# Kernel optimization log

Hardware: AMD Instinct MI355X
Metric: run time of the kernel (lower is better)

## Reference

```python
import jax, jax.numpy as jnp
import numpy as np


def setup_inputs() -> dict:
    key = jax.random.key(0)
    k1, k2 = jax.random.split(key)
    x = jax.random.normal(k1, (64, 64, 32, 32), dtype=jnp.float32)
    codebook = jax.random.normal(k2, (1024, 64), dtype=jnp.float32)
    return {"x": x, "codebook": codebook}


def reference(x, codebook):
    B, C, H, W = x.shape
    # NCHW -> NHWC -> [N, C] flat tokens
    xt = jnp.transpose(x, (0, 2, 3, 1)).reshape(-1, C)  # [N, C]
    # squared euclidean distances [N, K] (argmin of squared == argmin of cdist)
    x_sq = jnp.sum(xt * xt, axis=-1, keepdims=True)          # [N, 1]
    cb_sq = jnp.sum(codebook * codebook, axis=-1)            # [K]
    d2 = x_sq - 2.0 * (xt @ codebook.T) + cb_sq[None, :]     # [N, K]
    idx_emb = jnp.argmin(d2, axis=-1)                        # [N]
    quant = codebook[idx_emb]                                # [N, C]
    loss_embed = jnp.mean((jax.lax.stop_gradient(xt) - quant) ** 2)
    loss_commitment = jnp.mean((xt - jax.lax.stop_gradient(quant)) ** 2)
    # straight-through estimator
    quant_out = xt + jax.lax.stop_gradient(quant - xt)
    quant_out = quant_out.reshape(B, H, W, C).transpose(0, 3, 1, 2)
    idx_emb = idx_emb.reshape(B, H * W)
    return quant_out, loss_embed, loss_commitment, idx_emb
```

## Files before the change

kernel.cpp:

```cpp
#include <hip/hip_runtime.h>

#define THREADS 256
#define M_BLOCK 128
#define C_DIM 64
#define K_CODES 1024
#define N_CHUNK 64
#define N_CHUNKS 16

#define QUANT_OFF 0
#define LOSS_OFF  4194304
#define IDX_OFF   4194306

#define WS_CBSQH_F 16
#define WS_STREAM_B 8192
#define CHUNK_BYTES 24576
#define SEG_BYTES 1024
#define WS_NEEDED (WS_STREAM_B + N_CHUNKS * CHUNK_BYTES)

typedef float floatx16 __attribute__((ext_vector_type(16)));
typedef short bf16x8  __attribute__((ext_vector_type(8)));

typedef __attribute__((address_space(1))) const void gv_t;
typedef __attribute__((address_space(3))) void lv_t;

static __device__ inline unsigned short f2bf(float v) {
    unsigned int u = __float_as_uint(v);
    unsigned int r = (u + 0x7FFF + ((u >> 16) & 1)) >> 16;
    return (unsigned short)r;
}
static __device__ inline float bf2f(unsigned short b) {
    return __uint_as_float(((unsigned int)b) << 16);
}

__global__ void vq_prep(const float* __restrict__ cb, float* __restrict__ ws)
{
    const int tid = threadIdx.x;
    if (blockIdx.x >= 96) {
        int code = (blockIdx.x - 96) * 256 + tid;
        const float4* row = reinterpret_cast<const float4*>(cb + code * C_DIM);
        float s = 0.f;
        #pragma unroll
        for (int j = 0; j < 16; ++j) {
            float4 v = row[j];
            s = fmaf(v.x, v.x, s); s = fmaf(v.y, v.y, s);
            s = fmaf(v.z, v.z, s); s = fmaf(v.w, v.w, s);
        }
        ws[WS_CBSQH_F + code] = 0.5f * s;
        return;
    }
    int gid   = blockIdx.x * 256 + tid;
    int chunk = gid / 1536;
    int rem   = gid - chunk * 1536;
    int seg   = rem >> 6;
    int lane  = rem & 63;
    int wc = seg / 12;
    int tb = (seg % 12) >> 2;
    int s4 = seg & 3;
    int code = chunk * N_CHUNK + wc * 32 + (lane & 31);
    int c0   = s4 * 16 + ((lane >> 5) << 3);
    const float* src = cb + code * C_DIM + c0;
    unsigned short us[8];
    #pragma unroll
    for (int j = 0; j < 8; ++j) {
        float v  = src[j];
        float h  = bf2f(f2bf(v));
        float r1 = v - h;
        float m  = bf2f(f2bf(r1));
        float r2 = r1 - m;
        float sel = (tb == 0) ? h : (tb == 1) ? m : r2;
        us[j] = f2bf(-sel);
    }
    uint4 o;
    o.x = (unsigned)us[0] | ((unsigned)us[1] << 16);
    o.y = (unsigned)us[2] | ((unsigned)us[3] << 16);
    o.z = (unsigned)us[4] | ((unsigned)us[5] << 16);
    o.w = (unsigned)us[6] | ((unsigned)us[7] << 16);
    *reinterpret_cast<uint4*>((char*)ws + WS_STREAM_B + chunk * CHUNK_BYTES
                              + seg * SEG_BYTES + lane * 16) = o;
}

__global__ __launch_bounds__(THREADS, 2) void vq_main(
    const float* __restrict__ x,
    const float* __restrict__ cb,
    const float* __restrict__ ws_f,
    float* __restrict__ out,
    double* __restrict__ ws_sum)
{
    __shared__ __align__(16) char smem[49152];
    __shared__ float cbsqh_s[K_CODES];
    __shared__ float redv[2][M_BLOCK];
    __shared__ int   redi[2][M_BLOCK];
    __shared__ int   kidx_s[M_BLOCK];

    const int tid  = threadIdx.x;
    const int blk  = blockIdx.x;
    const int tok0 = blk * M_BLOCK;
    const int b    = tok0 >> 10;
    const int hw0  = tok0 & 1023;

    const int w   = tid >> 6;
    const int ln  = tid & 63;
    const int wr  = w >> 1;
    const int wc  = w & 1;
    const int l31 = ln & 31;
    const int l5  = ln >> 5;

    float* xs = reinterpret_cast<float*>(smem);
    #pragma unroll
    for (int j = 0; j < 32; ++j) {
        int idx = j * 256 + tid;
        int c = idx >> 7, t = idx & 127;
        xs[c * 130 + t] = x[((b * C_DIM + c) << 10) + hw0 + t];
    }
    #pragma unroll
    for (int r = 0; r < 4; ++r) {
        int q = r * 256 + tid;
        cbsqh_s[q] = ws_f[WS_CBSQH_F + q];
    }
    __syncthreads();

    bf16x8 afrag[2][3][4];
    #pragma unroll
    for (int mt = 0; mt < 2; ++mt) {
        const int token = wr * 64 + mt * 32 + l31;
        #pragma unroll
        for (int s4 = 0; s4 < 4; ++s4) {
            const int cb0 = s4 * 16 + l5 * 8;
            #pragma unroll
            for (int j = 0; j < 8; ++j) {
                float v  = xs[(cb0 + j) * 130 + token];
                float h  = bf2f(f2bf(v));
                float r1 = v - h;
                float m  = bf2f(f2bf(r1));
                float r2 = r1 - m;
                afrag[mt][0][s4][j] = (short)f2bf(h);
                afrag[mt][1][s4][j] = (short)f2bf(m);
                afrag[mt][2][s4][j] = (short)f2bf(r2);
            }
        }
    }
    __syncthreads();

    const char* stream = (const char*)ws_f + WS_STREAM_B;

    {
        char* buf = smem;
        #pragma unroll
        for (int it = 0; it < 6; ++it) {
            int seg = w * 6 + it;
            const char* g = stream + 0 * CHUNK_BYTES + seg * SEG_BYTES + ln * 16;
            __builtin_amdgcn_global_load_lds((gv_t*)g, (lv_t*)(buf + seg * SEG_BYTES), 16, 0, 0);
        }
    }
    __syncthreads();

    float minv[2][16];
    int   mini[2][16];
    #pragma unroll
    for (int mt = 0; mt < 2; ++mt)
        #pragma unroll
        for (int r = 0; r < 16; ++r) { minv[mt][r] = 3.4e38f; mini[mt][r] = 0; }

    for (int ch = 0; ch < N_CHUNKS; ++ch) {
        if (ch < N_CHUNKS - 1) {
            char* nbuf = smem + ((ch + 1) & 1) * CHUNK_BYTES;
            #pragma unroll
            for (int it = 0; it < 6; ++it) {
                int seg = w * 6 + it;
                const char* g = stream + (ch + 1) * CHUNK_BYTES + seg * SEG_BYTES + ln * 16;
                __builtin_amdgcn_global_load_lds((gv_t*)g, (lv_t*)(nbuf + seg * SEG_BYTES), 16, 0, 0);
            }
        }

        const char* bbase = smem + (ch & 1) * CHUNK_BYTES;
        const float h = cbsqh_s[ch * N_CHUNK + wc * 32 + l31];
        floatx16 acc0, acc1;
        #pragma unroll
        for (int r = 0; r < 16; ++r) { acc0[r] = h; acc1[r] = h; }

        #pragma unroll
        for (int tb = 0; tb < 3; ++tb) {
            #pragma unroll
            for (int s4 = 0; s4 < 4; ++s4) {
                bf16x8 bf = *reinterpret_cast<const bf16x8*>(
                    bbase + ((wc * 3 + tb) * 4 + s4) * SEG_BYTES + ln * 16);
                #pragma unroll
                for (int a = 0; a < 3; ++a) {
                    if (a + tb <= 2) {
                        acc0 = __builtin_amdgcn_mfma_f32_32x32x16_bf16(afrag[0][a][s4], bf, acc0, 0, 0, 0);
                        acc1 = __builtin_amdgcn_mfma_f32_32x32x16_bf16(afrag[1][a][s4], bf, acc1, 0, 0, 0);
                    }
                }
            }
        }

        const int idxc = ch * N_CHUNK + wc * 32 + l31;
        #pragma unroll
        for (int r = 0; r < 16; ++r) {
            float s0 = acc0[r];
            if (s0 < minv[0][r]) { minv[0][r] = s0; mini[0][r] = idxc; }
            float s1 = acc1[r];
            if (s1 < minv[1][r]) { minv[1][r] = s1; mini[1][r] = idxc; }
        }
        __syncthreads();
    }

    #pragma unroll
    for (int off = 1; off < 32; off <<= 1) {
        #pragma unroll
        for (int mt = 0; mt < 2; ++mt)
            #pragma unroll
            for (int r = 0; r < 16; ++r) {
                float ov = __shfl_xor(minv[mt][r], off, 64);
                int   oi = __shfl_xor(mini[mt][r], off, 64);
                if (ov < minv[mt][r] || (ov == minv[mt][r] && oi < mini[mt][r])) {
                    minv[mt][r] = ov; mini[mt][r] = oi;
                }
            }
    }
    if (l31 == 0) {
        #pragma unroll
        for (int mt = 0; mt < 2; ++mt)
            #pragma unroll
            for (int r = 0; r < 16; ++r) {
                int row = (r & 3) + ((r >> 2) << 3) + (l5 << 2);
                int token = wr * 64 + mt * 32 + row;
                redv[wc][token] = minv[mt][r];
                redi[wc][token] = mini[mt][r];
            }
    }
    __syncthreads();

    if (tid < M_BLOCK) {
        float v0 = redv[0][tid]; int i0 = redi[0][tid];
        float v1 = redv[1][tid]; int i1 = redi[1][tid];
        int bi = (v1 < v0 || (v1 == v0 && i1 < i0)) ? i1 : i0;
        kidx_s[tid] = bi;
        out[IDX_OFF + tok0 + tid] = (float)bi;
    }
    __syncthreads();

    {
        const int i  = tid & (M_BLOCK - 1);
        const int c0 = tid >> 7;
        const int kk = kidx_s[i];
        const float* crow = cb + kk * C_DIM;
        float lsum = 0.f;
        #pragma unroll
        for (int j = 0; j < 32; ++j) {
            int c = c0 * 32 + j;
            float q  = crow[c];
            float xv = x[((b * C_DIM + c) << 10) + hw0 + i];
            float d  = q - xv;
            lsum = fmaf(d, d, lsum);
            out[QUANT_OFF + ((b * C_DIM + c) << 10) + hw0 + i] = xv + d;
        }
        #pragma unroll
        for (int off = 32; off > 0; off >>= 1)
            lsum += __shfl_down(lsum, off, 64);
        if ((tid & 63) == 0)
            atomicAdd(ws_sum, (double)lsum);
    }
}

#define CB_PAD 68
__global__ __launch_bounds__(THREADS, 2) void vq_main_valu(
    const float* __restrict__ x,
    const float* __restrict__ cb,
    float* __restrict__ out,
    double* __restrict__ ws_sum)
{
    __shared__ float xt_s[C_DIM][M_BLOCK];
    __shared__ float cb_s[C_DIM][CB_PAD];
    __shared__ float cbsq_all[K_CODES];
    __shared__ float red_v[8][M_BLOCK];
    __shared__ int   red_i[8][M_BLOCK];
    __shared__ int   kidx_s[M_BLOCK];

    const int tid  = threadIdx.x;
    const int tok0 = blockIdx.x * M_BLOCK;
    const int b_img = tok0 >> 10;
    const int hw0   = tok0 & 1023;

    #pragma unroll
    for (int r = 0; r < 4; ++r) {
        int k = tid + r * THREADS;
        const float4* row = reinterpret_cast<const float4*>(cb + k * C_DIM);
        float s = 0.f;
        #pragma unroll
        for (int j = 0; j < 16; ++j) {
            float4 v = row[j];
            s = fmaf(v.x, v.x, s); s = fmaf(v.y, v.y, s);
            s = fmaf(v.z, v.z, s); s = fmaf(v.w, v.w, s);
        }
        cbsq_all[k] = s;
    }
    {
        const int i  = tid & (M_BLOCK - 1);
        const int c0 = tid >> 7;
        #pragma unroll
        for (int j = 0; j < 32; ++j) {
            int c = c0 + 2 * j;
            xt_s[c][i] = x[((b_img * C_DIM + c) << 10) + hw0 + i];
        }
    }

    const int tl = tid & 31;
    const int kg = tid >> 5;
    float minv[4]; int mini[4];
    #pragma unroll
    for (int m = 0; m < 4; ++m) { minv[m] = 3.4e38f; mini[m] = 0; }

    for (int ch = 0; ch < 16; ++ch) {
        __syncthreads();
        for (int t = tid; t < 64 * C_DIM; t += THREADS) {
            int kl = t >> 6, c = t & 63;
            cb_s[c][kl] = cb[(ch * 64 + kl) * C_DIM + c];
        }
        __syncthreads();
        float dot[4][8];
        #pragma unroll
        for (int m = 0; m < 4; ++m)
            #pragma unroll
            for (int k = 0; k < 8; ++k) dot[m][k] = 0.f;
        #pragma unroll 4
        for (int c = 0; c < C_DIM; ++c) {
            float4 xv  = *reinterpret_cast<const float4*>(&xt_s[c][tl * 4]);
            float4 cv0 = *reinterpret_cast<const float4*>(&cb_s[c][kg * 8]);
            float4 cv1 = *reinterpret_cast<const float4*>(&cb_s[c][kg * 8 + 4]);
            float xa[4] = {xv.x, xv.y, xv.z, xv.w};
            float ca[8] = {cv0.x, cv0.y, cv0.z, cv0.w, cv1.x, cv1.y, cv1.z, cv1.w};
            #pragma unroll
            for (int m = 0; m < 4; ++m)
                #pragma unroll
                for (int k = 0; k < 8; ++k)
                    dot[m][k] = fmaf(xa[m], ca[k], dot[m][k]);
        }
        const int codebase = ch * 64 + kg * 8;
        #pragma unroll
        for (int k = 0; k < 8; ++k) {
            float csq = cbsq_all[codebase + k];
            #pragma unroll
            for (int m = 0; m < 4; ++m) {
                float sc = fmaf(-2.f, dot[m][k], csq);
                if (sc < minv[m]) { minv[m] = sc; mini[m] = codebase + k; }
            }
        }
    }
    #pragma unroll
    for (int m = 0; m < 4; ++m) {
        red_v[kg][tl * 4 + m] = minv[m];
        red_i[kg][tl * 4 + m] = mini[m];
    }
    __syncthreads();
    if (tid < M_BLOCK) {
        float bv = red_v[0][tid]; int bi = red_i[0][tid];
        #pragma unroll
        for (int g = 1; g < 8; ++g) {
            float v = red_v[g][tid]; int ii = red_i[g][tid];
            if (v < bv || (v == bv && ii < bi)) { bv = v; bi = ii; }
        }
        kidx_s[tid] = bi;
        out[IDX_OFF + tok0 + tid] = (float)bi;
    }
    __syncthreads();
    {
        const int i  = tid & (M_BLOCK - 1);
        const int c0 = tid >> 7;
        const int kk = kidx_s[i];
        const float* crow = cb + kk * C_DIM;
        float lsum = 0.f;
        #pragma unroll
        for (int j = 0; j < 32; ++j) {
            int c = c0 * 32 + j;
            float q  = crow[c];
            float xv = xt_s[c][i];
            float d  = q - xv;
            lsum = fmaf(d, d, lsum);
            out[QUANT_OFF + ((b_img * C_DIM + c) << 10) + hw0 + i] = xv + d;
        }
        #pragma unroll
        for (int off = 32; off > 0; off >>= 1)
            lsum += __shfl_down(lsum, off, 64);
        if ((tid & 63) == 0)
            atomicAdd(ws_sum, (double)lsum);
    }
}

__global__ void vq_finalize(const double* __restrict__ ws_sum,
                            float* __restrict__ out)
{
    float m = (float)(ws_sum[0] / 4194304.0);
    out[LOSS_OFF]     = m;
    out[LOSS_OFF + 1] = m;
}

extern "C" void kernel_launch(void* const* d_in, const int* in_sizes, int n_in,
                              void* d_out, int out_size, void* d_ws, size_t ws_size,
                              hipStream_t stream) {
    const float* x  = (const float*)d_in[0];
    const float* cb = (const float*)d_in[1];
    float* out      = (float*)d_out;

    hipMemsetAsync(d_ws, 0, sizeof(double), stream);
    if (ws_size >= (size_t)WS_NEEDED) {
        vq_prep<<<100, THREADS, 0, stream>>>(cb, (float*)d_ws);
        vq_main<<<512, THREADS, 0, stream>>>(x, cb, (const float*)d_ws, out, (double*)d_ws);
    } else {
        vq_main_valu<<<512, THREADS, 0, stream>>>(x, cb, out, (double*)d_ws);
    }
    vq_finalize<<<1, 1, 0, stream>>>((const double*)d_ws, out);
}
```

Before: 147.5 us.

## Stream codebook fragments directly to registers and drop LDS double buffering

The main kernel no longer stages codebook chunks in LDS through global_load_lds with per-chunk barriers. Each wave now loads its B fragments straight from global memory into registers, using two register sets (bA/bB) that are software-pipelined across pairs of chunks. The epilogue reads x from the retained LDS tile instead of re-reading global memory, and the prep kernel is relaunched with 64-thread blocks. This removes LDS traffic and block-wide syncs, but it adds register pressure (24 extra bf16x8 vectors) that may hurt occupancy at 2 waves/SIMD, and it relies on L2 for codebook reuse.

```diff
diff --git a/kernel.cpp b/kernel.cpp
--- a/kernel.cpp
+++ b/kernel.cpp
@@ -20,9 +20,6 @@
 typedef float floatx16 __attribute__((ext_vector_type(16)));
 typedef short bf16x8  __attribute__((ext_vector_type(8)));
 
-typedef __attribute__((address_space(1))) const void gv_t;
-typedef __attribute__((address_space(3))) void lv_t;
-
 static __device__ inline unsigned short f2bf(float v) {
     unsigned int u = __float_as_uint(v);
     unsigned int r = (u + 0x7FFF + ((u >> 16) & 1)) >> 16;
@@ -35,8 +32,9 @@
 __global__ void vq_prep(const float* __restrict__ cb, float* __restrict__ ws)
 {
     const int tid = threadIdx.x;
-    if (blockIdx.x >= 96) {
-        int code = (blockIdx.x - 96) * 256 + tid;
+    const int blk = blockIdx.x;
+    if (blk >= 384) {
+        int code = (blk - 384) * 64 + tid;
         const float4* row = reinterpret_cast<const float4*>(cb + code * C_DIM);
         float s = 0.f;
         #pragma unroll
@@ -48,16 +46,14 @@
         ws[WS_CBSQH_F + code] = 0.5f * s;
         return;
     }
-    int gid   = blockIdx.x * 256 + tid;
-    int chunk = gid / 1536;
-    int rem   = gid - chunk * 1536;
-    int seg   = rem >> 6;
-    int lane  = rem & 63;
-    int wc = seg / 12;
-    int tb = (seg % 12) >> 2;
-    int s4 = seg & 3;
-    int code = chunk * N_CHUNK + wc * 32 + (lane & 31);
-    int c0   = s4 * 16 + ((lane >> 5) << 3);
+    const int chunk = blk / 24;
+    const int seg   = blk - chunk * 24;
+    const int wc = seg / 12;
+    const int r12 = seg - wc * 12;
+    const int tb = r12 >> 2;
+    const int s4 = seg & 3;
+    const int code = chunk * N_CHUNK + wc * 32 + (tid & 31);
+    const int c0   = s4 * 16 + ((tid >> 5) << 3);
     const float* src = cb + code * C_DIM + c0;
     unsigned short us[8];
     #pragma unroll
@@ -76,7 +72,7 @@
     o.z = (unsigned)us[4] | ((unsigned)us[5] << 16);
     o.w = (unsigned)us[6] | ((unsigned)us[7] << 16);
     *reinterpret_cast<uint4*>((char*)ws + WS_STREAM_B + chunk * CHUNK_BYTES
-                              + seg * SEG_BYTES + lane * 16) = o;
+                              + seg * SEG_BYTES + tid * 16) = o;
 }
 
 __global__ __launch_bounds__(THREADS, 2) void vq_main(
@@ -86,15 +82,14 @@
     float* __restrict__ out,
     double* __restrict__ ws_sum)
 {
-    __shared__ __align__(16) char smem[49152];
+    __shared__ __align__(16) float xs[C_DIM * 130];
     __shared__ float cbsqh_s[K_CODES];
     __shared__ float redv[2][M_BLOCK];
     __shared__ int   redi[2][M_BLOCK];
     __shared__ int   kidx_s[M_BLOCK];
 
     const int tid  = threadIdx.x;
-    const int blk  = blockIdx.x;
-    const int tok0 = blk * M_BLOCK;
+    const int tok0 = blockIdx.x * M_BLOCK;
     const int b    = tok0 >> 10;
     const int hw0  = tok0 & 1023;
 
@@ -105,7 +100,6 @@
     const int l31 = ln & 31;
     const int l5  = ln >> 5;
 
-    float* xs = reinterpret_cast<float*>(smem);
     #pragma unroll
     for (int j = 0; j < 32; ++j) {
         int idx = j * 256 + tid;
@@ -139,20 +133,8 @@
             }
         }
     }
-    __syncthreads();
-
-    const char* stream = (const char*)ws_f + WS_STREAM_B;
-
-    {
-        char* buf = smem;
-        #pragma unroll
-        for (int it = 0; it < 6; ++it) {
-            int seg = w * 6 + it;
-            const char* g = stream + 0 * CHUNK_BYTES + seg * SEG_BYTES + ln * 16;
-            __builtin_amdgcn_global_load_lds((gv_t*)g, (lv_t*)(buf + seg * SEG_BYTES), 16, 0, 0);
-        }
-    }
-    __syncthreads();
+
+    const char* wbase = (const char*)ws_f + WS_STREAM_B + wc * 12 * SEG_BYTES + ln * 16;
 
     float minv[2][16];
     int   mini[2][16];
@@ -161,48 +143,74 @@
         #pragma unroll
         for (int r = 0; r < 16; ++r) { minv[mt][r] = 3.4e38f; mini[mt][r] = 0; }
 
-    for (int ch = 0; ch < N_CHUNKS; ++ch) {
-        if (ch < N_CHUNKS - 1) {
-            char* nbuf = smem + ((ch + 1) & 1) * CHUNK_BYTES;
-            #pragma unroll
-            for (int it = 0; it < 6; ++it) {
-                int seg = w * 6 + it;
-                const char* g = stream + (ch + 1) * CHUNK_BYTES + seg * SEG_BYTES + ln * 16;
-                __builtin_amdgcn_global_load_lds((gv_t*)g, (lv_t*)(nbuf + seg * SEG_BYTES), 16, 0, 0);
-            }
-        }
-
-        const char* bbase = smem + (ch & 1) * CHUNK_BYTES;
-        const float h = cbsqh_s[ch * N_CHUNK + wc * 32 + l31];
-        floatx16 acc0, acc1;
-        #pragma unroll
-        for (int r = 0; r < 16; ++r) { acc0[r] = h; acc1[r] = h; }
-
-        #pragma unroll
-        for (int tb = 0; tb < 3; ++tb) {
-            #pragma unroll
-            for (int s4 = 0; s4 < 4; ++s4) {
-                bf16x8 bf = *reinterpret_cast<const bf16x8*>(
-                    bbase + ((wc * 3 + tb) * 4 + s4) * SEG_BYTES + ln * 16);
+    bf16x8 bA[12], bB[12];
+
+    #pragma unroll
+    for (int t = 0; t < 12; ++t)
+        bA[t] = *reinterpret_cast<const bf16x8*>(wbase + 0 * CHUNK_BYTES + t * SEG_BYTES);
+
+    #pragma unroll 1
+    for (int ch = 0; ch < N_CHUNKS; ch += 2) {
+        #pragma unroll
+        for (int t = 0; t < 12; ++t)
+            bB[t] = *reinterpret_cast<const bf16x8*>(wbase + (ch + 1) * CHUNK_BYTES + t * SEG_BYTES);
+
+        {
+            const float h = cbsqh_s[ch * N_CHUNK + wc * 32 + l31];
+            floatx16 acc0, acc1;
+            #pragma unroll
+            for (int r = 0; r < 16; ++r) { acc0[r] = h; acc1[r] = h; }
+            #pragma unroll
+            for (int tb = 0; tb < 3; ++tb)
                 #pragma unroll
-                for (int a = 0; a < 3; ++a) {
-                    if (a + tb <= 2) {
-                        acc0 = __builtin_amdgcn_mfma_f32_32x32x16_bf16(afrag[0][a][s4], bf, acc0, 0, 0, 0);
-                        acc1 = __builtin_amdgcn_mfma_f32_32x32x16_bf16(afrag[1][a][s4], bf, acc1, 0, 0, 0);
-                    }
+                for (int s4 = 0; s4 < 4; ++s4) {
+                    bf16x8 bf = bA[tb * 4 + s4];
+                    #pragma unroll
+                    for (int a = 0; a < 3; ++a)
+                        if (a + tb <= 2) {
+                            acc0 = __builtin_amdgcn_mfma_f32_32x32x16_bf16(afrag[0][a][s4], bf, acc0, 0, 0, 0);
+                            acc1 = __builtin_amdgcn_mfma_f32_32x32x16_bf16(afrag[1][a][s4], bf, acc1, 0, 0, 0);
+                        }
                 }
-            }
-        }
-
-        const int idxc = ch * N_CHUNK + wc * 32 + l31;
-        #pragma unroll
-        for (int r = 0; r < 16; ++r) {
-            float s0 = acc0[r];
-            if (s0 < minv[0][r]) { minv[0][r] = s0; mini[0][r] = idxc; }
-            float s1 = acc1[r];
-            if (s1 < minv[1][r]) { minv[1][r] = s1; mini[1][r] = idxc; }
-        }
-        __syncthreads();
+            const int idxc = ch * N_CHUNK + wc * 32 + l31;
+            #pragma unroll
+            for (int r = 0; r < 16; ++r) {
+                if (acc0[r] < minv[0][r]) { minv[0][r] = acc0[r]; mini[0][r] = idxc; }
+                if (acc1[r] < minv[1][r]) { minv[1][r] = acc1[r]; mini[1][r] = idxc; }
+            }
+        }
+
+        {
+            const int pc = (ch + 2 > N_CHUNKS - 1) ? (N_CHUNKS - 1) : (ch + 2);
+            #pragma unroll
+            for (int t = 0; t < 12; ++t)
+                bA[t] = *reinterpret_cast<const bf16x8*>(wbase + pc * CHUNK_BYTES + t * SEG_BYTES);
+        }
+
+        {
+            const float h = cbsqh_s[(ch + 1) * N_CHUNK + wc * 32 + l31];
+            floatx16 acc0, acc1;
+            #pragma unroll
+            for (int r = 0; r < 16; ++r) { acc0[r] = h; acc1[r] = h; }
+            #pragma unroll
+            for (int tb = 0; tb < 3; ++tb)
+                #pragma unroll
+                for (int s4 = 0; s4 < 4; ++s4) {
+                    bf16x8 bf = bB[tb * 4 + s4];
+                    #pragma unroll
+                    for (int a = 0; a < 3; ++a)
+                        if (a + tb <= 2) {
+                            acc0 = __builtin_amdgcn_mfma_f32_32x32x16_bf16(afrag[0][a][s4], bf, acc0, 0, 0, 0);
+                            acc1 = __builtin_amdgcn_mfma_f32_32x32x16_bf16(afrag[1][a][s4], bf, acc1, 0, 0, 0);
+                        }
+                }
+            const int idxc = (ch + 1) * N_CHUNK + wc * 32 + l31;
+            #pragma unroll
+            for (int r = 0; r < 16; ++r) {
+                if (acc0[r] < minv[0][r]) { minv[0][r] = acc0[r]; mini[0][r] = idxc; }
+                if (acc1[r] < minv[1][r]) { minv[1][r] = acc1[r]; mini[1][r] = idxc; }
+            }
+        }
     }
 
     #pragma unroll
@@ -250,7 +258,7 @@
         for (int j = 0; j < 32; ++j) {
             int c = c0 * 32 + j;
             float q  = crow[c];
-            float xv = x[((b * C_DIM + c) << 10) + hw0 + i];
+            float xv = xs[c * 130 + i];
             float d  = q - xv;
             lsum = fmaf(d, d, lsum);
             out[QUANT_OFF + ((b * C_DIM + c) << 10) + hw0 + i] = xv + d;
@@ -404,7 +412,7 @@
 
     hipMemsetAsync(d_ws, 0, sizeof(double), stream);
     if (ws_size >= (size_t)WS_NEEDED) {
-        vq_prep<<<100, THREADS, 0, stream>>>(cb, (float*)d_ws);
+        vq_prep<<<400, 64, 0, stream>>>(cb, (float*)d_ws);
         vq_main<<<512, THREADS, 0, stream>>>(x, cb, (const float*)d_ws, out, (double*)d_ws);
     } else {
         vq_main_valu<<<512, THREADS, 0, stream>>>(x, cb, out, (double*)d_ws);
```

Measured after the change: 154.7 us. +4.9%, slower.

## Restructure MFMA VQ kernel to 512 threads with swapped operands and smaller per-wave tiles

Applied to the files above, without the earlier changes.

The main kernel moves to 512-thread blocks. Each wave handles 32 tokens by 32 codes, with codebook fragments as the A operand and token fragments as B. This lets each lane track a single running min, so the wide cross-lane shuffle reduction collapses to one xor step. Two independent accumulators split the MFMA dependency chain, the codebook-norm term is added after the MFMA instead of preloaded, and the prep kernel is re-laid out into 32-code chunks. The intent is to cut register pressure and reduction overhead and to raise occupancy, at the cost of more blocks' worth of LDS traffic per token.

```diff
diff --git a/kernel.cpp b/kernel.cpp
--- a/kernel.cpp
+++ b/kernel.cpp
@@ -1,11 +1,7 @@
 #include <hip/hip_runtime.h>
 
-#define THREADS 256
-#define M_BLOCK 128
 #define C_DIM 64
 #define K_CODES 1024
-#define N_CHUNK 64
-#define N_CHUNKS 16
 
 #define QUANT_OFF 0
 #define LOSS_OFF  4194304
@@ -13,8 +9,9 @@
 
 #define WS_CBSQH_F 16
 #define WS_STREAM_B 8192
-#define CHUNK_BYTES 24576
 #define SEG_BYTES 1024
+#define CHUNK_BYTES 12288
+#define N_CHUNKS 32
 #define WS_NEEDED (WS_STREAM_B + N_CHUNKS * CHUNK_BYTES)
 
 typedef float floatx16 __attribute__((ext_vector_type(16)));
@@ -35,8 +32,9 @@
 __global__ void vq_prep(const float* __restrict__ cb, float* __restrict__ ws)
 {
     const int tid = threadIdx.x;
-    if (blockIdx.x >= 96) {
-        int code = (blockIdx.x - 96) * 256 + tid;
+    const int blk = blockIdx.x;
+    if (blk >= 384) {
+        int code = (blk - 384) * 64 + tid;
         const float4* row = reinterpret_cast<const float4*>(cb + code * C_DIM);
         float s = 0.f;
         #pragma unroll
@@ -48,16 +46,12 @@
         ws[WS_CBSQH_F + code] = 0.5f * s;
         return;
     }
-    int gid   = blockIdx.x * 256 + tid;
-    int chunk = gid / 1536;
-    int rem   = gid - chunk * 1536;
-    int seg   = rem >> 6;
-    int lane  = rem & 63;
-    int wc = seg / 12;
-    int tb = (seg % 12) >> 2;
-    int s4 = seg & 3;
-    int code = chunk * N_CHUNK + wc * 32 + (lane & 31);
-    int c0   = s4 * 16 + ((lane >> 5) << 3);
+    const int chunk = blk / 12;
+    const int seg   = blk - chunk * 12;
+    const int tb = seg >> 2;
+    const int s4 = seg & 3;
+    const int code = chunk * 32 + (tid & 31);
+    const int c0   = s4 * 16 + ((tid >> 5) << 3);
     const float* src = cb + code * C_DIM + c0;
     unsigned short us[8];
     #pragma unroll
@@ -76,10 +70,10 @@
     o.z = (unsigned)us[4] | ((unsigned)us[5] << 16);
     o.w = (unsigned)us[6] | ((unsigned)us[7] << 16);
     *reinterpret_cast<uint4*>((char*)ws + WS_STREAM_B + chunk * CHUNK_BYTES
-                              + seg * SEG_BYTES + lane * 16) = o;
-}
-
-__global__ __launch_bounds__(THREADS, 2) void vq_main(
+                              + seg * SEG_BYTES + tid * 16) = o;
+}
+
+__global__ __launch_bounds__(512, 4) void vq_main(
     const float* __restrict__ x,
     const float* __restrict__ cb,
     const float* __restrict__ ws_f,
@@ -88,41 +82,36 @@
 {
     __shared__ __align__(16) char smem[49152];
     __shared__ float cbsqh_s[K_CODES];
-    __shared__ float redv[2][M_BLOCK];
-    __shared__ int   redi[2][M_BLOCK];
-    __shared__ int   kidx_s[M_BLOCK];
+    __shared__ float redv[2][128];
+    __shared__ int   redi[2][128];
+    __shared__ int   kidx_s[128];
 
     const int tid  = threadIdx.x;
-    const int blk  = blockIdx.x;
-    const int tok0 = blk * M_BLOCK;
+    const int tok0 = blockIdx.x * 128;
     const int b    = tok0 >> 10;
     const int hw0  = tok0 & 1023;
 
     const int w   = tid >> 6;
     const int ln  = tid & 63;
-    const int wr  = w >> 1;
-    const int wc  = w & 1;
+    const int tw  = w >> 1;
+    const int kw  = w & 1;
     const int l31 = ln & 31;
     const int l5  = ln >> 5;
 
     float* xs = reinterpret_cast<float*>(smem);
     #pragma unroll
-    for (int j = 0; j < 32; ++j) {
-        int idx = j * 256 + tid;
+    for (int j = 0; j < 16; ++j) {
+        int idx = j * 512 + tid;
         int c = idx >> 7, t = idx & 127;
         xs[c * 130 + t] = x[((b * C_DIM + c) << 10) + hw0 + t];
     }
-    #pragma unroll
-    for (int r = 0; r < 4; ++r) {
-        int q = r * 256 + tid;
-        cbsqh_s[q] = ws_f[WS_CBSQH_F + q];
-    }
-    __syncthreads();
-
-    bf16x8 afrag[2][3][4];
-    #pragma unroll
-    for (int mt = 0; mt < 2; ++mt) {
-        const int token = wr * 64 + mt * 32 + l31;
+    cbsqh_s[tid]       = ws_f[WS_CBSQH_F + tid];
+    cbsqh_s[tid + 512] = ws_f[WS_CBSQH_F + tid + 512];
+    __syncthreads();
+
+    bf16x8 tf[3][4];
+    {
+        const int token = tw * 32 + l31;
         #pragma unroll
         for (int s4 = 0; s4 < 4; ++s4) {
             const int cb0 = s4 * 16 + l5 * 8;
@@ -133,9 +122,9 @@
                 float r1 = v - h;
                 float m  = bf2f(f2bf(r1));
                 float r2 = r1 - m;
-                afrag[mt][0][s4][j] = (short)f2bf(h);
-                afrag[mt][1][s4][j] = (short)f2bf(m);
-                afrag[mt][2][s4][j] = (short)f2bf(r2);
+                tf[0][s4][j] = (short)f2bf(h);
+                tf[1][s4][j] = (short)f2bf(m);
+                tf[2][s4][j] = (short)f2bf(r2);
             }
         }
     }
@@ -143,95 +132,88 @@
 
     const char* stream = (const char*)ws_f + WS_STREAM_B;
 
-    {
-        char* buf = smem;
-        #pragma unroll
-        for (int it = 0; it < 6; ++it) {
-            int seg = w * 6 + it;
-            const char* g = stream + 0 * CHUNK_BYTES + seg * SEG_BYTES + ln * 16;
-            __builtin_amdgcn_global_load_lds((gv_t*)g, (lv_t*)(buf + seg * SEG_BYTES), 16, 0, 0);
-        }
-    }
-    __syncthreads();
-
-    float minv[2][16];
-    int   mini[2][16];
-    #pragma unroll
-    for (int mt = 0; mt < 2; ++mt)
-        #pragma unroll
-        for (int r = 0; r < 16; ++r) { minv[mt][r] = 3.4e38f; mini[mt][r] = 0; }
-
-    for (int ch = 0; ch < N_CHUNKS; ++ch) {
-        if (ch < N_CHUNKS - 1) {
-            char* nbuf = smem + ((ch + 1) & 1) * CHUNK_BYTES;
-            #pragma unroll
-            for (int it = 0; it < 6; ++it) {
-                int seg = w * 6 + it;
-                const char* g = stream + (ch + 1) * CHUNK_BYTES + seg * SEG_BYTES + ln * 16;
-                __builtin_amdgcn_global_load_lds((gv_t*)g, (lv_t*)(nbuf + seg * SEG_BYTES), 16, 0, 0);
+    #pragma unroll
+    for (int it = 0; it < 3; ++it) {
+        int s  = w * 3 + it;
+        int p  = s / 12;
+        int si = s - p * 12;
+        const char* g = stream + p * CHUNK_BYTES + si * SEG_BYTES + ln * 16;
+        __builtin_amdgcn_global_load_lds((gv_t*)g,
+            (lv_t*)(smem + p * 24576 + si * SEG_BYTES + ln * 16), 16, 0, 0);
+    }
+    __syncthreads();
+
+    float minv = 3.4e38f;
+    int   mini = 0;
+
+    #pragma unroll 1
+    for (int i = 0; i < 16; ++i) {
+        if (i < 15) {
+            #pragma unroll
+            for (int it = 0; it < 3; ++it) {
+                int s  = w * 3 + it;
+                int p  = s / 12;
+                int si = s - p * 12;
+                const char* g = stream + (2 * (i + 1) + p) * CHUNK_BYTES + si * SEG_BYTES + ln * 16;
+                __builtin_amdgcn_global_load_lds((gv_t*)g,
+                    (lv_t*)(smem + p * 24576 + ((i + 1) & 1) * CHUNK_BYTES + si * SEG_BYTES + ln * 16),
+                    16, 0, 0);
             }
         }
 
-        const char* bbase = smem + (ch & 1) * CHUNK_BYTES;
-        const float h = cbsqh_s[ch * N_CHUNK + wc * 32 + l31];
-        floatx16 acc0, acc1;
-        #pragma unroll
-        for (int r = 0; r < 16; ++r) { acc0[r] = h; acc1[r] = h; }
+        const char* abase = smem + kw * 24576 + (i & 1) * CHUNK_BYTES;
+        floatx16 accA, accB;
+        #pragma unroll
+        for (int r = 0; r < 16; ++r) { accA[r] = 0.f; accB[r] = 0.f; }
 
         #pragma unroll
         for (int tb = 0; tb < 3; ++tb) {
             #pragma unroll
             for (int s4 = 0; s4 < 4; ++s4) {
-                bf16x8 bf = *reinterpret_cast<const bf16x8*>(
-                    bbase + ((wc * 3 + tb) * 4 + s4) * SEG_BYTES + ln * 16);
+                bf16x8 as = *reinterpret_cast<const bf16x8*>(
+                    abase + (tb * 4 + s4) * SEG_BYTES + ln * 16);
                 #pragma unroll
                 for (int a = 0; a < 3; ++a) {
                     if (a + tb <= 2) {
-                        acc0 = __builtin_amdgcn_mfma_f32_32x32x16_bf16(afrag[0][a][s4], bf, acc0, 0, 0, 0);
-                        acc1 = __builtin_amdgcn_mfma_f32_32x32x16_bf16(afrag[1][a][s4], bf, acc1, 0, 0, 0);
+                        if (((a + s4) & 1) == 0)
+                            accA = __builtin_amdgcn_mfma_f32_32x32x16_bf16(as, tf[a][s4], accA, 0, 0, 0);
+                        else
+                            accB = __builtin_amdgcn_mfma_f32_32x32x16_bf16(as, tf[a][s4], accB, 0, 0, 0);
                     }
                 }
             }
         }
 
-        const int idxc = ch * N_CHUNK + wc * 32 + l31;
+        const int chbase = (2 * i + kw) * 32;
+        const float* cp = &cbsqh_s[chbase + 4 * l5];
+        float4 cq0 = *reinterpret_cast<const float4*>(cp);
+        float4 cq1 = *reinterpret_cast<const float4*>(cp + 8);
+        float4 cq2 = *reinterpret_cast<const float4*>(cp + 16);
+        float4 cq3 = *reinterpret_cast<const float4*>(cp + 24);
+        float cqa[16] = {cq0.x, cq0.y, cq0.z, cq0.w, cq1.x, cq1.y, cq1.z, cq1.w,
+                         cq2.x, cq2.y, cq2.z, cq2.w, cq3.x, cq3.y, cq3.z, cq3.w};
         #pragma unroll
         for (int r = 0; r < 16; ++r) {
-            float s0 = acc0[r];
-            if (s0 < minv[0][r]) { minv[0][r] = s0; mini[0][r] = idxc; }
-            float s1 = acc1[r];
-            if (s1 < minv[1][r]) { minv[1][r] = s1; mini[1][r] = idxc; }
-        }
+            float v = accA[r] + accB[r] + cqa[r];
+            int idx = chbase + 8 * (r >> 2) + 4 * l5 + (r & 3);
+            if (v < minv) { minv = v; mini = idx; }
+        }
+
         __syncthreads();
     }
 
-    #pragma unroll
-    for (int off = 1; off < 32; off <<= 1) {
-        #pragma unroll
-        for (int mt = 0; mt < 2; ++mt)
-            #pragma unroll
-            for (int r = 0; r < 16; ++r) {
-                float ov = __shfl_xor(minv[mt][r], off, 64);
-                int   oi = __shfl_xor(mini[mt][r], off, 64);
-                if (ov < minv[mt][r] || (ov == minv[mt][r] && oi < mini[mt][r])) {
-                    minv[mt][r] = ov; mini[mt][r] = oi;
-                }
-            }
-    }
-    if (l31 == 0) {
-        #pragma unroll
-        for (int mt = 0; mt < 2; ++mt)
-            #pragma unroll
-            for (int r = 0; r < 16; ++r) {
-                int row = (r & 3) + ((r >> 2) << 3) + (l5 << 2);
-                int token = wr * 64 + mt * 32 + row;
-                redv[wc][token] = minv[mt][r];
-                redi[wc][token] = mini[mt][r];
-            }
-    }
-    __syncthreads();
-
-    if (tid < M_BLOCK) {
+    {
+        float ov = __shfl_xor(minv, 32, 64);
+        int   oi = __shfl_xor(mini, 32, 64);
+        if (ov < minv || (ov == minv && oi < mini)) { minv = ov; mini = oi; }
+        if (ln < 32) {
+            redv[kw][tw * 32 + ln] = minv;
+            redi[kw][tw * 32 + ln] = mini;
+        }
+    }
+    __syncthreads();
+
+    if (tid < 128) {
         float v0 = redv[0][tid]; int i0 = redi[0][tid];
         float v1 = redv[1][tid]; int i1 = redi[1][tid];
         int bi = (v1 < v0 || (v1 == v0 && i1 < i0)) ? i1 : i0;
@@ -241,14 +223,14 @@
     __syncthreads();
 
     {
-        const int i  = tid & (M_BLOCK - 1);
+        const int i  = tid & 127;
         const int c0 = tid >> 7;
         const int kk = kidx_s[i];
         const float* crow = cb + kk * C_DIM;
         float lsum = 0.f;
         #pragma unroll
-        for (int j = 0; j < 32; ++j) {
-            int c = c0 * 32 + j;
+        for (int j = 0; j < 16; ++j) {
+            int c = c0 * 16 + j;
             float q  = crow[c];
             float xv = x[((b * C_DIM + c) << 10) + hw0 + i];
             float d  = q - xv;
@@ -264,27 +246,27 @@
 }
 
 #define CB_PAD 68
-__global__ __launch_bounds__(THREADS, 2) void vq_main_valu(
+__global__ __launch_bounds__(256, 2) void vq_main_valu(
     const float* __restrict__ x,
     const float* __restrict__ cb,
     float* __restrict__ out,
     double* __restrict__ ws_sum)
 {
-    __shared__ float xt_s[C_DIM][M_BLOCK];
+    __shared__ float xt_s[C_DIM][128];
     __shared__ float cb_s[C_DIM][CB_PAD];
     __shared__ float cbsq_all[K_CODES];
-    __shared__ float red_v[8][M_BLOCK];
-    __shared__ int   red_i[8][M_BLOCK];
-    __shared__ int   kidx_s[M_BLOCK];
+    __shared__ float red_v[8][128];
+    __shared__ int   red_i[8][128];
+    __shared__ int   kidx_s[128];
 
     const int tid  = threadIdx.x;
-    const int tok0 = blockIdx.x * M_BLOCK;
+    const int tok0 = blockIdx.x * 128;
     const int b_img = tok0 >> 10;
     const int hw0   = tok0 & 1023;
 
     #pragma unroll
     for (int r = 0; r < 4; ++r) {
-        int k = tid + r * THREADS;
+        int k = tid + r * 256;
         const float4* row = reinterpret_cast<const float4*>(cb + k * C_DIM);
         float s = 0.f;
         #pragma unroll
@@ -296,7 +278,7 @@
         cbsq_all[k] = s;
     }
     {
-        const int i  = tid & (M_BLOCK - 1);
+        const int i  = tid & 127;
         const int c0 = tid >> 7;
         #pragma unroll
         for (int j = 0; j < 32; ++j) {
@@ -313,7 +295,7 @@
 
     for (int ch = 0; ch < 16; ++ch) {
         __syncthreads();
-        for (int t = tid; t < 64 * C_DIM; t += THREADS) {
+        for (int t = tid; t < 64 * C_DIM; t += 256) {
             int kl = t >> 6, c = t & 63;
             cb_s[c][kl] = cb[(ch * 64 + kl) * C_DIM + c];
         }
@@ -353,7 +335,7 @@
         red_i[kg][tl * 4 + m] = mini[m];
     }
     __syncthreads();
-    if (tid < M_BLOCK) {
+    if (tid < 128) {
         float bv = red_v[0][tid]; int bi = red_i[0][tid];
         #pragma unroll
         for (int g = 1; g < 8; ++g) {
@@ -365,7 +347,7 @@
     }
     __syncthreads();
     {
-        const int i  = tid & (M_BLOCK - 1);
+        const int i  = tid & 127;
         const int c0 = tid >> 7;
         const int kk = kidx_s[i];
         const float* crow = cb + kk * C_DIM;
@@ -404,10 +386,10 @@
 
     hipMemsetAsync(d_ws, 0, sizeof(double), stream);
     if (ws_size >= (size_t)WS_NEEDED) {
-        vq_prep<<<100, THREADS, 0, stream>>>(cb, (float*)d_ws);
-        vq_main<<<512, THREADS, 0, stream>>>(x, cb, (const float*)d_ws, out, (double*)d_ws);
+        vq_prep<<<400, 64, 0, stream>>>(cb, (float*)d_ws);
+        vq_main<<<512, 512, 0, stream>>>(x, cb, (const float*)d_ws, out, (double*)d_ws);
     } else {
-        vq_main_valu<<<512, THREADS, 0, stream>>>(x, cb, out, (double*)d_ws);
+        vq_main_valu<<<512, 256, 0, stream>>>(x, cb, out, (double*)d_ws);
     }
     vq_finalize<<<1, 1, 0, stream>>>((const double*)d_ws, out);
 }
```

Measured after the change: 160.0 us. +8.5%, slower.
